# Kernel optimization log

Hardware: AMD Instinct MI355X
Metric: run time of the kernel (lower is better)

Reference implementation:

```python
import jax, jax.numpy as jnp
import numpy as np

CORNER_MASK = jnp.array(
    [[0, 0, 0], [0, 0, 1], [0, 1, 0], [0, 1, 1],
     [1, 0, 0], [1, 0, 1], [1, 1, 0], [1, 1, 1]], dtype=jnp.float32)


def setup_inputs() -> dict:
    key = jax.random.key(0)
    k1, k2, k3, k4 = jax.random.split(key, 4)
    DEPTH = 6
    G = 2 ** DEPTH            # 64 voxels per axis at depth 6
    C = 32                    # feature channels
    H = G * G * G             # 262144 octree nodes at depth 6
    N = 1_000_000             # query points (depth-7 node centers)

    data = jax.random.normal(k1, (1, C, H, 1), dtype=jnp.float32)
    # points scaled into [0, 2^depth]; last column is the batch id (single octree -> 0)
    xyz = jax.random.uniform(k2, (N, 3), dtype=jnp.float32) * G
    ids = jnp.zeros((N, 1), dtype=jnp.float32)
    pts = jnp.concatenate([xyz, ids], axis=1)

    # dense voxel -> node-index lookup emulating ocnn.octree_search_key;
    idx_grid = jax.random.randint(k3, (G, G, G), 0, H, dtype=jnp.int32)
    empty = jax.random.uniform(k4, (G, G, G)) < 0.1
    lut = jnp.where(empty, jnp.int32(-1), idx_grid)

    return {"data": data, "pts": pts, "lut": lut, "depth": DEPTH}


def reference(data, pts, lut, depth):
    # data: (1, C, H, 1); pts: (N, 4); lut: (G, G, G) int32; depth: python int
    G = 2 ** depth
    xyzf = pts[:, :3] - 0.5                      # (N, 3)
    xyzi = jnp.floor(xyzf)
    frac = xyzf - xyzi                           # (N, 3) fractional offsets

    corners = xyzi[:, None, :] + CORNER_MASK[None, :, :]   # (N, 8, 3)
    ci = corners.astype(jnp.int32)
    in_bounds = jnp.all((ci >= 0) & (ci < G), axis=-1)     # (N, 8)
    ci_safe = jnp.clip(ci, 0, G - 1)
    idx = lut[ci_safe[..., 0], ci_safe[..., 1], ci_safe[..., 2]]  # (N, 8)
    valid = in_bounds & (idx > -1)

    # trilinear weights: |prod((1 - mask) - frac)|, matching the torch code
    w = jnp.abs(jnp.prod((1.0 - CORNER_MASK)[None, :, :] - frac[:, None, :], axis=-1))
    w = jnp.where(valid, w, 0.0)                 # (N, 8)
    idx_safe = jnp.where(valid, idx, 0)

    feat = data[0, :, :, 0].T                    # (H, C)
    gathered = feat[idx_safe]                    # (N, 8, C)
    out = jnp.einsum('nk,nkc->nc', w, gathered)  # weighted accumulate
    norm = jnp.sum(w, axis=1, keepdims=True)     # (N, 1)
    out = out / (norm + 1e-10)
    return out.T[None, :, :, None]               # (1, C, N, 1)
```

## Files before the change

kernel.cpp:

```cpp
#include <hip/hip_runtime.h>
#include <hip/hip_fp16.h>


#define NCH 32
#define BIN_W 512
#define NGRP 8
#define CAP 128

typedef float nvec4 __attribute__((ext_vector_type(4)));

__global__ __launch_bounds__(256) void octri_pre1(
    const float* __restrict__ data, __half* __restrict__ featH, int H, int TB,
    const float* __restrict__ pts, int N, int NB, float* __restrict__ binned,
    int* __restrict__ inv, int* __restrict__ cnt) {
  __shared__ float tile[32][33];
  __shared__ int lcnt[NGRP];
  __shared__ int wbase[4][NGRP];
  const int t = threadIdx.x;

  if ((int)blockIdx.x < TB) {
    const int h0 = blockIdx.x * 32;
    const int tx = t & 31, ty = t >> 5;
#pragma unroll
    for (int i = 0; i < 4; ++i) {
      int c = ty + 8 * i;
      tile[c][tx] = __builtin_nontemporal_load(&data[(size_t)c * H + h0 + tx]);
    }
    __syncthreads();
#pragma unroll
    for (int i = 0; i < 4; ++i) {
      int hl = ty + 8 * i;
      featH[(size_t)(h0 + hl) * NCH + tx] = __float2half(tile[tx][hl]);
    }
  } else {
    const int b = blockIdx.x - TB;
    const int lane = t & 63, wid = t >> 6;
    if (t < NGRP) lcnt[t] = 0;
    __syncthreads();
#pragma unroll
    for (int i = 0; i < 2; ++i) {
      const int n = b * BIN_W + i * 256 + t;
      const bool act = (n < N);
      nvec4 pt = {0.f, 0.f, 0.f, 0.f};
      int g = 0;
      if (act) {
        pt = __builtin_nontemporal_load((const nvec4*)(pts + (size_t)n * 4));
        g = min(max((int)floorf(pt.x - 0.5f), 0), 63) >> 3;
      }
      unsigned long long m = 0;
#pragma unroll
      for (int gg = 0; gg < NGRP; ++gg) {
        const unsigned long long bm = __ballot(act && (g == gg));
        if (gg == g) m = bm;
      }
      const unsigned long long ltm = (1ull << lane) - 1ull;
      const int rank = __popcll(m & ltm);
      if (act && rank == 0) wbase[wid][g] = atomicAdd(&lcnt[g], __popcll(m));
      __syncthreads();
      if (act) {
        const int rtot = wbase[wid][g] + rank;
        const int rk = min(rtot, CAP - 1);
        const int slot = ((g * NB + b) << 7) + rk;
        if (rtot < CAP)
          __builtin_nontemporal_store(pt, (nvec4*)(binned + (size_t)slot * 4));
        inv[n] = (g << 28) | slot;
      }
      __syncthreads();
    }
    if (t < NGRP) cnt[t * NB + b] = min(lcnt[t], CAP);
  }
}

__global__ __launch_bounds__(256) void octri_voxelize(
    const __half* __restrict__ featH, const int* __restrict__ lut,
    __half* __restrict__ featV, unsigned long long* __restrict__ vmask) {
  const int t = threadIdx.x;
  const int zi = t >> 2;
  const int j = t & 3;
  const int v = blockIdx.x * 64 + zi;
  const int id = __builtin_nontemporal_load(&lut[v]);

  nvec4 row = {0.f, 0.f, 0.f, 0.f};
  if (id >= 0)
    row = __builtin_nontemporal_load(
        (const nvec4*)(featH + ((size_t)id << 5) + (j << 3)));
  *(nvec4*)(featV + ((size_t)v << 5) + (j << 3)) = row;

  const unsigned long long b = __ballot(id >= 0);
  unsigned int comp = 0;
#pragma unroll
  for (int k = 0; k < 16; ++k)
    comp |= ((unsigned)(b >> (4 * k)) & 1u) << k;
  __shared__ unsigned short sm16[4];
  if ((t & 63) == 0) sm16[t >> 6] = (unsigned short)comp;
  __syncthreads();
  if (t == 0) {
    unsigned long long m = (unsigned long long)sm16[0] |
                           ((unsigned long long)sm16[1] << 16) |
                           ((unsigned long long)sm16[2] << 32) |
                           ((unsigned long long)sm16[3] << 48);
    vmask[blockIdx.x] = m;
  }
}

__global__ __launch_bounds__(256) void octri_gather5(
    const __half* __restrict__ featV, const unsigned long long* __restrict__ vmask,
    const float* __restrict__ binned, const int* __restrict__ cnt, int NB,
    __half* __restrict__ temp) {
  __shared__ int meta[256][17];
  __shared__ int scnt[2];
  const int g = blockIdx.x & 7;
  const int b0 = (blockIdx.x >> 3) << 1;
  const int t = threadIdx.x;

  if (t < 2) scnt[t] = (b0 + t < NB) ? cnt[g * NB + b0 + t] : 0;
  __syncthreads();

  {
    const int r = t >> 7, off = t & 127;
    const int wofs = (t >> 6) & 1;
    if ((wofs << 6) < scnt[r]) {
      const bool valid = off < scnt[r];
      const int slot = ((g * NB + (b0 + r)) << 7) + off;
      nvec4 pt = {0.f, 0.f, 0.f, 0.f};
      if (valid)
        pt = __builtin_nontemporal_load(
            (const nvec4*)(binned + (size_t)slot * 4));
      const float fx = pt.x - 0.5f, fy = pt.y - 0.5f, fz = pt.z - 0.5f;
      const float flx = floorf(fx), fly = floorf(fy), flz = floorf(fz);
      const int ix = (int)flx, iy = (int)fly, iz = (int)flz;
      const float rx = fx - flx, ry = fy - fly, rz = fz - flz;
      const float wx[2] = {1.f - rx, rx};
      const float wy[2] = {1.f - ry, ry};
      const float wz[2] = {1.f - rz, rz};
      const bool vx[2] = {(unsigned)ix < 64u, (unsigned)(ix + 1) < 64u};
      const bool vy[2] = {(unsigned)iy < 64u, (unsigned)(iy + 1) < 64u};
      const bool vz[2] = {(unsigned)iz < 64u, (unsigned)(iz + 1) < 64u};
      const int cxc[2] = {min(max(ix, 0), 63), min(max(ix + 1, 0), 63)};
      const int cyc[2] = {min(max(iy, 0), 63), min(max(iy + 1, 0), 63)};
      const int czc[2] = {min(max(iz, 0), 63), min(max(iz + 1, 0), 63)};

      unsigned long long mrow[2][2];
#pragma unroll
      for (int bx = 0; bx < 2; ++bx)
#pragma unroll
        for (int by = 0; by < 2; ++by)
          mrow[bx][by] = vmask[(cxc[bx] << 6) + cyc[by]];

      int vv[8];
      float w[8], wsum = 0.f;
#pragma unroll
      for (int k = 0; k < 8; ++k) {
        const int bx = (k >> 2) & 1, by = (k >> 1) & 1, bz = k & 1;
        const bool ok = vx[bx] && vy[by] && vz[bz] &&
                        (((mrow[bx][by] >> czc[bz]) & 1ull) != 0);
        vv[k] = ((cxc[bx] << 6) + cyc[by]) * 64 + czc[bz];
        float wk = wx[bx] * wy[by] * wz[bz];
        wk = ok ? wk : 0.f;
        w[k] = wk;
        wsum += wk;
      }
      const float sc = valid ? (1.f / (wsum + 1e-10f)) : 0.f;
#pragma unroll
      for (int k = 0; k < 8; ++k) {
        meta[t][k] = vv[k];
        meta[t][8 + k] = __float_as_int(w[k] * sc);
      }
    }
  }
  __syncthreads();

  const int lane = t & 63;
  const int wid = t >> 6;
  const int j = lane & 3;
  const int sc = scnt[wid >> 1];
#pragma unroll
  for (int gq = 0; gq < 4; ++gq) {
    const int base = ((wid & 1) << 6) + (gq << 4);
    if (base >= sc) break;
    const int p = (wid << 6) + (gq << 4) + (lane >> 2);

    nvec4 r[8];
    float ws[8];
#pragma unroll
    for (int k = 0; k < 8; ++k) {
      const int v = meta[p][k];
      ws[k] = __int_as_float(meta[p][8 + k]);
      r[k] = *(const nvec4*)(featV + ((size_t)v << 5) + (j << 3));
    }
    float acc[8] = {};
#pragma unroll
    for (int k = 0; k < 8; ++k) {
      const __half2* h2 = (const __half2*)&r[k];
#pragma unroll
      for (int q = 0; q < 4; ++q) {
        const float2 f = __half22float2(h2[q]);
        acc[2 * q + 0] += ws[k] * f.x;
        acc[2 * q + 1] += ws[k] * f.y;
      }
    }
    if ((p & 127) < sc) {
      const int slot = ((g * NB + (b0 + (p >> 7))) << 7) + (p & 127);
      union { __half2 h2[4]; nvec4 v; } u;
#pragma unroll
      for (int q = 0; q < 4; ++q)
        u.h2[q] = __floats2half2_rn(acc[2 * q], acc[2 * q + 1]);
      __builtin_nontemporal_store(
          u.v, (nvec4*)(temp + ((size_t)slot << 5) + (j << 3)));
    }
  }
}

__global__ __launch_bounds__(256) void octri_unpermute2(
    const __half* __restrict__ temp, const int* __restrict__ inv,
    const int* __restrict__ cnt, int NB, int N, float* __restrict__ out) {
  __shared__ __half rows[BIN_W * NCH];
  __shared__ int cnt8[NGRP], pre[NGRP];
  const int b = blockIdx.x;
  const int t = threadIdx.x;
  if (t < NGRP) cnt8[t] = cnt[t * NB + b];
  __syncthreads();
  if (t == 0) {
    int s = 0;
#pragma unroll
    for (int gg = 0; gg < NGRP; ++gg) { pre[gg] = s; s += cnt8[gg]; }
  }
  __syncthreads();
  for (int gg = 0; gg < NGRP; ++gg) {
    const int len4 = cnt8[gg] << 2;
    const __half* src = temp + ((size_t)((gg * NB + b)) << 12);
    const int rbase = pre[gg];
    for (int k = t; k < len4; k += 256) {
      const int row = k >> 2, e = k & 3;
      const nvec4 v = __builtin_nontemporal_load(
          (const nvec4*)(src + ((size_t)row << 5) + (e << 3)));
      const int r = rbase + row;
      *(nvec4*)(rows + ((size_t)r << 5) + ((e ^ (r & 3)) << 3)) = v;
    }
  }
  __syncthreads();
#pragma unroll
  for (int i = 0; i < 2; ++i) {
    const int n = b * BIN_W + i * 256 + t;
    if (n < N) {
      const int iv = inv[n];
      const int g = ((unsigned)iv) >> 28;
      const int r = pre[g] + (iv & (CAP - 1));
      const __half* hp = rows + ((size_t)r << 5);
#pragma unroll
      for (int k = 0; k < 4; ++k) {
        const nvec4 hv = *(const nvec4*)(hp + ((k ^ (r & 3)) << 3));
        const __half2* h2 = (const __half2*)&hv;
#pragma unroll
        for (int q = 0; q < 4; ++q) {
          const float2 f = __half22float2(h2[q]);
          __builtin_nontemporal_store(f.x,
                                      &out[(size_t)(k * 8 + 2 * q) * N + n]);
          __builtin_nontemporal_store(
              f.y, &out[(size_t)(k * 8 + 2 * q + 1) * N + n]);
        }
      }
    }
  }
}

__global__ __launch_bounds__(256) void octri_transpose_h(
    const float* __restrict__ data, __half* __restrict__ featH, int H) {
  __shared__ float tile[32][33];
  const int h0 = blockIdx.x * 32;
  const int tx = threadIdx.x;
  const int ty = threadIdx.y;
#pragma unroll
  for (int i = 0; i < 4; ++i) {
    int c = ty + 8 * i;
    tile[c][tx] = __builtin_nontemporal_load(&data[(size_t)c * H + h0 + tx]);
  }
  __syncthreads();
#pragma unroll
  for (int i = 0; i < 4; ++i) {
    int hl = ty + 8 * i;
    featH[(size_t)(h0 + hl) * NCH + tx] = __float2half(tile[tx][hl]);
  }
}

__global__ __launch_bounds__(256) void octri_gather3(
    const __half* __restrict__ featV, const unsigned long long* __restrict__ vmask,
    const float* __restrict__ pts, const int* __restrict__ depth_p,
    float* __restrict__ out, int N) {
  __shared__ int meta[256][17];
  const int pblk = blockIdx.x * 256;
  const int G = 1 << depth_p[0];
  const int G1 = G - 1;
  {
    const int p = threadIdx.x;
    const int n = min(pblk + p, N - 1);
    const nvec4 pt =
        __builtin_nontemporal_load((const nvec4*)(pts + (size_t)n * 4));
    const float fx = pt.x - 0.5f, fy = pt.y - 0.5f, fz = pt.z - 0.5f;
    const float flx = floorf(fx), fly = floorf(fy), flz = floorf(fz);
    const int ix = (int)flx, iy = (int)fly, iz = (int)flz;
    const float rx = fx - flx, ry = fy - fly, rz = fz - flz;
    const float wx[2] = {1.f - rx, rx};
    const float wy[2] = {1.f - ry, ry};
    const float wz[2] = {1.f - rz, rz};
    const bool vx[2] = {(unsigned)ix < (unsigned)G,
                        (unsigned)(ix + 1) < (unsigned)G};
    const bool vy[2] = {(unsigned)iy < (unsigned)G,
                        (unsigned)(iy + 1) < (unsigned)G};
    const bool vz[2] = {(unsigned)iz < (unsigned)G,
                        (unsigned)(iz + 1) < (unsigned)G};
    const int cxc[2] = {min(max(ix, 0), G1), min(max(ix + 1, 0), G1)};
    const int cyc[2] = {min(max(iy, 0), G1), min(max(iy + 1, 0), G1)};
    const int czc[2] = {min(max(iz, 0), G1), min(max(iz + 1, 0), G1)};
    unsigned long long mrow[2][2];
#pragma unroll
    for (int bx = 0; bx < 2; ++bx)
#pragma unroll
      for (int by = 0; by < 2; ++by)
        mrow[bx][by] = vmask[cxc[bx] * G + cyc[by]];
    int vv[8];
    float w[8], wsum = 0.f;
#pragma unroll
    for (int k = 0; k < 8; ++k) {
      const int bx = (k >> 2) & 1, by = (k >> 1) & 1, bz = k & 1;
      const bool valid = vx[bx] && vy[by] && vz[bz] &&
                         (((mrow[bx][by] >> czc[bz]) & 1ull) != 0);
      vv[k] = (cxc[bx] * G + cyc[by]) * G + czc[bz];
      float wk = wx[bx] * wy[by] * wz[bz];
      wk = valid ? wk : 0.f;
      w[k] = wk;
      wsum += wk;
    }
    const float s = (pblk + p < N) ? (1.f / (wsum + 1e-10f)) : 0.f;
#pragma unroll
    for (int k = 0; k < 8; ++k) {
      meta[p][k] = vv[k];
      meta[p][8 + k] = __float_as_int(w[k] * s);
    }
  }
  __syncthreads();
  const int lane = threadIdx.x & 63;
  const int wid = threadIdx.x >> 6;
  const int j = lane & 3;
#pragma unroll
  for (int g = 0; g < 4; ++g) {
    const int p = (wid << 6) + (g << 4) + (lane >> 2);
    const int n = pblk + p;
    nvec4 r[8];
    float ws[8];
#pragma unroll
    for (int k = 0; k < 8; ++k) {
      const int v = meta[p][k];
      ws[k] = __int_as_float(meta[p][8 + k]);
      r[k] = *(const nvec4*)(featV + ((size_t)v << 5) + (j << 3));
    }
    float acc[8] = {};
#pragma unroll
    for (int k = 0; k < 8; ++k) {
      const __half2* h2 = (const __half2*)&r[k];
#pragma unroll
      for (int q = 0; q < 4; ++q) {
        const float2 f = __half22float2(h2[q]);
        acc[2 * q + 0] += ws[k] * f.x;
        acc[2 * q + 1] += ws[k] * f.y;
      }
    }
    if (n < N) {
#pragma unroll
      for (int q = 0; q < 8; ++q)
        __builtin_nontemporal_store(acc[q], &out[(size_t)(8 * j + q) * N + n]);
    }
  }
}

__global__ __launch_bounds__(256) void octri_gather_direct(
    const float* __restrict__ data, const float* __restrict__ pts,
    const int* __restrict__ lut, const int* __restrict__ depth_p,
    float* __restrict__ out, int N, int H) {
  const int n = blockIdx.x * blockDim.x + threadIdx.x;
  if (n >= N) return;
  const int G = 1 << depth_p[0];
  const float4 p = ((const float4*)pts)[n];
  const float fx = p.x - 0.5f, fy = p.y - 0.5f, fz = p.z - 0.5f;
  const float flx = floorf(fx), fly = floorf(fy), flz = floorf(fz);
  const int ix = (int)flx, iy = (int)fly, iz = (int)flz;
  const float rx = fx - flx, ry = fy - fly, rz = fz - flz;
  const float wx[2] = {1.f - rx, rx};
  const float wy[2] = {1.f - ry, ry};
  const float wz[2] = {1.f - rz, rz};
  int idx[8];
  float w[8], wsum = 0.f;
#pragma unroll
  for (int k = 0; k < 8; ++k) {
    const int bx = (k >> 2) & 1, by = (k >> 1) & 1, bz = k & 1;
    const int cx = ix + bx, cy = iy + by, cz = iz + bz;
    const bool inb = (cx >= 0) & (cx < G) & (cy >= 0) & (cy < G) & (cz >= 0) &
                     (cz < G);
    int id = -1;
    if (inb) id = lut[((size_t)cx * G + cy) * G + cz];
    const bool valid = inb && (id > -1);
    float wk = wx[bx] * wy[by] * wz[bz];
    wk = valid ? wk : 0.f;
    idx[k] = valid ? id : 0;
    w[k] = wk;
    wsum += wk;
  }
  const float s = 1.f / (wsum + 1e-10f);
#pragma unroll 4
  for (int c = 0; c < NCH; ++c) {
    const float* plane = data + (size_t)c * H;
    float a = 0.f;
#pragma unroll
    for (int k = 0; k < 8; ++k) a += w[k] * plane[idx[k]];
    out[(size_t)c * N + n] = a * s;
  }
}

extern "C" void kernel_launch(void* const* d_in, const int* in_sizes, int n_in,
                              void* d_out, int out_size, void* d_ws,
                              size_t ws_size, hipStream_t stream) {
  const float* data = (const float*)d_in[0];
  const float* pts = (const float*)d_in[1];
  const int* lut = (const int*)d_in[2];
  const int* depth_p = (const int*)d_in[3];
  float* out = (float*)d_out;

  const int H = in_sizes[0] / NCH;
  const int N = in_sizes[1] / 4;
  const int SV = in_sizes[2];

  int G = 1;
  while ((size_t)(G + 1) * (G + 1) * (G + 1) <= (size_t)SV) ++G;

  const int NB = (N + BIN_W - 1) / BIN_W;

  const size_t featH_bytes = (size_t)H * NCH * sizeof(__half);
  const size_t featV_bytes = (size_t)SV * NCH * sizeof(__half);
  const size_t nslots = (size_t)NGRP * NB * CAP;

  size_t offw = 0;
  auto alloc = [&](size_t bytes) {
    offw = (offw + 255) & ~(size_t)255;
    size_t o = offw;
    offw += bytes;
    return o;
  };
  const size_t o_featH = alloc(featH_bytes);
  const size_t o_featV = alloc(featV_bytes);
  const size_t o_vmask = alloc((size_t)G * G * sizeof(unsigned long long));
  const size_t o_binned = alloc(nslots * 16);
  const size_t o_temp = alloc(nslots * NCH * sizeof(__half));
  const size_t o_inv = alloc((size_t)NB * BIN_W * sizeof(int));
  const size_t o_cnt = alloc((size_t)NGRP * NB * sizeof(int));
  const size_t need_full = offw;

  const size_t needV = featV_bytes + (size_t)G * G * sizeof(unsigned long long);

  if (G == 64 && (size_t)G * G * G == (size_t)SV && (H % 32) == 0 &&
      nslots < (1u << 21) && ws_size >= need_full) {
    char* ws = (char*)d_ws;
    __half* featH = (__half*)(ws + o_featH);
    __half* featV = (__half*)(ws + o_featV);
    unsigned long long* vmask = (unsigned long long*)(ws + o_vmask);
    float* binned = (float*)(ws + o_binned);
    __half* temp = (__half*)(ws + o_temp);
    int* inv = (int*)(ws + o_inv);
    int* cnt = (int*)(ws + o_cnt);

    const int TB = H / 32;
    octri_pre1<<<TB + NB, 256, 0, stream>>>(data, featH, H, TB, pts, N, NB,
                                            binned, inv, cnt);
    octri_voxelize<<<SV / 64, 256, 0, stream>>>(featH, lut, featV, vmask);
    const int PB = (NB + 1) >> 1;
    octri_gather5<<<NGRP * PB, 256, 0, stream>>>(featV, vmask, binned, cnt,
                                                 NB, temp);
    octri_unpermute2<<<NB, 256, 0, stream>>>(temp, inv, cnt, NB, N, out);
  } else if (G == 64 && (size_t)G * G * G == (size_t)SV && (H % 32) == 0 &&
             ws_size >= needV &&
             featH_bytes <= (size_t)out_size * sizeof(float)) {
    __half* featH = (__half*)d_out;
    __half* featV = (__half*)d_ws;
    unsigned long long* vmask =
        (unsigned long long*)((char*)d_ws + featV_bytes);
    dim3 tb(32, 8);
    octri_transpose_h<<<H / 32, tb, 0, stream>>>(data, featH, H);
    octri_voxelize<<<SV / 64, 256, 0, stream>>>(featH, lut, featV, vmask);
    octri_gather3<<<(N + 255) / 256, 256, 0, stream>>>(featV, vmask, pts,
                                                       depth_p, out, N);
  } else {
    octri_gather_direct<<<(N + 255) / 256, 256, 0, stream>>>(
        data, pts, lut, depth_p, out, N, H);
  }
}
```

Baseline: 258.2 us.

## Fuse four pipeline kernels into one cooperative persistent kernel with grid syncs

Replaces the four separate launches (transpose+binning, voxelize, gather, unpermute) with a single cooperative kernel that runs the stages as grid-stride loops separated by grid.sync(). The aim is to remove per-kernel launch and drain gaps between stages. The grid is sized from occupancy times CU count. The old kernel sequence stays as a fallback if the cooperative launch fails, and the unused three-kernel path is removed. In exchange, grid-wide barriers are added, and the persistent grid may give lower occupancy or worse load balance than the original launches.

```diff
diff --git a/kernel.cpp b/kernel.cpp
--- a/kernel.cpp
+++ b/kernel.cpp
@@ -1,5 +1,8 @@
 #include <hip/hip_runtime.h>
 #include <hip/hip_fp16.h>
+#include <hip/hip_cooperative_groups.h>
+
+namespace cg = cooperative_groups;
 
 
 #define NCH 32
@@ -8,6 +11,271 @@
 #define CAP 128
 
 typedef float nvec4 __attribute__((ext_vector_type(4)));
+
+__global__ __launch_bounds__(256) void octri_fused(
+    const float* __restrict__ data, const int* __restrict__ lut,
+    const float* __restrict__ pts, __half* __restrict__ featH,
+    __half* __restrict__ featV, unsigned long long* __restrict__ vmask,
+    float* __restrict__ binned, int* __restrict__ inv, int* __restrict__ cnt,
+    __half* __restrict__ temp, float* __restrict__ out, int H, int N, int NB,
+    int TB, int SVB) {
+  __shared__ alignas(16) char sm[32896];
+  float(*tile)[33] = (float(*)[33])sm;
+  int* lcnt = (int*)sm;
+  int(*wbase)[NGRP] = (int(*)[NGRP])(sm + 64);
+  unsigned short* sm16 = (unsigned short*)sm;
+  int(*meta)[17] = (int(*)[17])sm;
+  int* scnt = (int*)(sm + 17408);
+  __half* rows = (__half*)sm;
+  int* cnt8 = (int*)(sm + 32768);
+  int* pre = (int*)(sm + 32800);
+
+  const int t = threadIdx.x;
+  const int nblk = gridDim.x;
+  cg::grid_group grid = cg::this_grid();
+
+  for (int bt = blockIdx.x; bt < TB; bt += nblk) {
+    const int h0 = bt * 32;
+    const int tx = t & 31, ty = t >> 5;
+#pragma unroll
+    for (int i = 0; i < 4; ++i) {
+      int c = ty + 8 * i;
+      tile[c][tx] =
+          __builtin_nontemporal_load(&data[(size_t)c * H + h0 + tx]);
+    }
+    __syncthreads();
+#pragma unroll
+    for (int i = 0; i < 4; ++i) {
+      int hl = ty + 8 * i;
+      featH[(size_t)(h0 + hl) * NCH + tx] = __float2half(tile[tx][hl]);
+    }
+    __syncthreads();
+  }
+  for (int b = blockIdx.x; b < NB; b += nblk) {
+    const int lane = t & 63, wid = t >> 6;
+    if (t < NGRP) lcnt[t] = 0;
+    __syncthreads();
+#pragma unroll
+    for (int i = 0; i < 2; ++i) {
+      const int n = b * BIN_W + i * 256 + t;
+      const bool act = (n < N);
+      nvec4 pt = {0.f, 0.f, 0.f, 0.f};
+      int g = 0;
+      if (act) {
+        pt = __builtin_nontemporal_load((const nvec4*)(pts + (size_t)n * 4));
+        g = min(max((int)floorf(pt.x - 0.5f), 0), 63) >> 3;
+      }
+      unsigned long long m = 0;
+#pragma unroll
+      for (int gg = 0; gg < NGRP; ++gg) {
+        const unsigned long long bm = __ballot(act && (g == gg));
+        if (gg == g) m = bm;
+      }
+      const unsigned long long ltm = (1ull << lane) - 1ull;
+      const int rank = __popcll(m & ltm);
+      if (act && rank == 0) wbase[wid][g] = atomicAdd(&lcnt[g], __popcll(m));
+      __syncthreads();
+      if (act) {
+        const int rtot = wbase[wid][g] + rank;
+        const int rk = min(rtot, CAP - 1);
+        const int slot = ((g * NB + b) << 7) + rk;
+        if (rtot < CAP)
+          __builtin_nontemporal_store(pt,
+                                      (nvec4*)(binned + (size_t)slot * 4));
+        inv[n] = (g << 28) | slot;
+      }
+      __syncthreads();
+    }
+    if (t < NGRP) cnt[t * NB + b] = min(lcnt[t], CAP);
+    __syncthreads();
+  }
+  grid.sync();
+
+  for (int vb = blockIdx.x; vb < SVB; vb += nblk) {
+    const int zi = t >> 2, j = t & 3;
+    const int v = vb * 64 + zi;
+    const int id = __builtin_nontemporal_load(&lut[v]);
+    nvec4 row = {0.f, 0.f, 0.f, 0.f};
+    if (id >= 0)
+      row = __builtin_nontemporal_load(
+          (const nvec4*)(featH + ((size_t)id << 5) + (j << 3)));
+    *(nvec4*)(featV + ((size_t)v << 5) + (j << 3)) = row;
+
+    const unsigned long long bb = __ballot(id >= 0);
+    unsigned int comp = 0;
+#pragma unroll
+    for (int k = 0; k < 16; ++k)
+      comp |= ((unsigned)(bb >> (4 * k)) & 1u) << k;
+    if ((t & 63) == 0) sm16[t >> 6] = (unsigned short)comp;
+    __syncthreads();
+    if (t == 0) {
+      unsigned long long m = (unsigned long long)sm16[0] |
+                             ((unsigned long long)sm16[1] << 16) |
+                             ((unsigned long long)sm16[2] << 32) |
+                             ((unsigned long long)sm16[3] << 48);
+      vmask[vb] = m;
+    }
+    __syncthreads();
+  }
+  grid.sync();
+
+  {
+    const int g = blockIdx.x & 7;
+    const int PBtot = (NB + 1) >> 1;
+    for (int pb = blockIdx.x >> 3; pb < PBtot; pb += (nblk >> 3)) {
+      const int b0 = pb << 1;
+      if (t < 2) scnt[t] = (b0 + t < NB) ? cnt[g * NB + b0 + t] : 0;
+      __syncthreads();
+      {
+        const int r = t >> 7, off = t & 127;
+        const int wofs = (t >> 6) & 1;
+        if ((wofs << 6) < scnt[r]) {
+          const bool valid = off < scnt[r];
+          const int slot = ((g * NB + (b0 + r)) << 7) + off;
+          nvec4 pt = {0.f, 0.f, 0.f, 0.f};
+          if (valid)
+            pt = __builtin_nontemporal_load(
+                (const nvec4*)(binned + (size_t)slot * 4));
+          const float fx = pt.x - 0.5f, fy = pt.y - 0.5f, fz = pt.z - 0.5f;
+          const float flx = floorf(fx), fly = floorf(fy), flz = floorf(fz);
+          const int ix = (int)flx, iy = (int)fly, iz = (int)flz;
+          const float rx = fx - flx, ry = fy - fly, rz = fz - flz;
+          const float wx[2] = {1.f - rx, rx};
+          const float wy[2] = {1.f - ry, ry};
+          const float wz[2] = {1.f - rz, rz};
+          const bool vx[2] = {(unsigned)ix < 64u, (unsigned)(ix + 1) < 64u};
+          const bool vy[2] = {(unsigned)iy < 64u, (unsigned)(iy + 1) < 64u};
+          const bool vz[2] = {(unsigned)iz < 64u, (unsigned)(iz + 1) < 64u};
+          const int cxc[2] = {min(max(ix, 0), 63), min(max(ix + 1, 0), 63)};
+          const int cyc[2] = {min(max(iy, 0), 63), min(max(iy + 1, 0), 63)};
+          const int czc[2] = {min(max(iz, 0), 63), min(max(iz + 1, 0), 63)};
+          unsigned long long mrow[2][2];
+#pragma unroll
+          for (int bx = 0; bx < 2; ++bx)
+#pragma unroll
+            for (int by = 0; by < 2; ++by)
+              mrow[bx][by] = vmask[(cxc[bx] << 6) + cyc[by]];
+          int vv[8];
+          float w[8], wsum = 0.f;
+#pragma unroll
+          for (int k = 0; k < 8; ++k) {
+            const int bx = (k >> 2) & 1, by = (k >> 1) & 1, bz = k & 1;
+            const bool ok = vx[bx] && vy[by] && vz[bz] &&
+                            (((mrow[bx][by] >> czc[bz]) & 1ull) != 0);
+            vv[k] = ((cxc[bx] << 6) + cyc[by]) * 64 + czc[bz];
+            float wk = wx[bx] * wy[by] * wz[bz];
+            wk = ok ? wk : 0.f;
+            w[k] = wk;
+            wsum += wk;
+          }
+          const float sc0 = valid ? (1.f / (wsum + 1e-10f)) : 0.f;
+#pragma unroll
+          for (int k = 0; k < 8; ++k) {
+            meta[t][k] = vv[k];
+            meta[t][8 + k] = __float_as_int(w[k] * sc0);
+          }
+        }
+      }
+      __syncthreads();
+      {
+        const int lane = t & 63;
+        const int wid = t >> 6;
+        const int j = lane & 3;
+        const int sc2 = scnt[wid >> 1];
+#pragma unroll
+        for (int gq = 0; gq < 4; ++gq) {
+          const int base = ((wid & 1) << 6) + (gq << 4);
+          if (base >= sc2) break;
+          const int p = (wid << 6) + (gq << 4) + (lane >> 2);
+          nvec4 r[8];
+          float ws[8];
+#pragma unroll
+          for (int k = 0; k < 8; ++k) {
+            const int v = meta[p][k];
+            ws[k] = __int_as_float(meta[p][8 + k]);
+            r[k] = *(const nvec4*)(featV + ((size_t)v << 5) + (j << 3));
+          }
+          float acc[8] = {};
+#pragma unroll
+          for (int k = 0; k < 8; ++k) {
+            const __half2* h2 = (const __half2*)&r[k];
+#pragma unroll
+            for (int q = 0; q < 4; ++q) {
+              const float2 f = __half22float2(h2[q]);
+              acc[2 * q + 0] += ws[k] * f.x;
+              acc[2 * q + 1] += ws[k] * f.y;
+            }
+          }
+          if ((p & 127) < sc2) {
+            const int slot = ((g * NB + (b0 + (p >> 7))) << 7) + (p & 127);
+            union {
+              __half2 h2[4];
+              nvec4 v;
+            } u;
+#pragma unroll
+            for (int q = 0; q < 4; ++q)
+              u.h2[q] = __floats2half2_rn(acc[2 * q], acc[2 * q + 1]);
+            __builtin_nontemporal_store(
+                u.v, (nvec4*)(temp + ((size_t)slot << 5) + (j << 3)));
+          }
+        }
+      }
+      __syncthreads();
+    }
+  }
+  grid.sync();
+
+  for (int b = blockIdx.x; b < NB; b += nblk) {
+    if (t < NGRP) cnt8[t] = cnt[t * NB + b];
+    __syncthreads();
+    if (t == 0) {
+      int s = 0;
+#pragma unroll
+      for (int gg = 0; gg < NGRP; ++gg) {
+        pre[gg] = s;
+        s += cnt8[gg];
+      }
+    }
+    __syncthreads();
+    for (int gg = 0; gg < NGRP; ++gg) {
+      const int len4 = cnt8[gg] << 2;
+      const __half* src = temp + ((size_t)(gg * NB + b) << 12);
+      const int rbase = pre[gg];
+      for (int k = t; k < len4; k += 256) {
+        const int row = k >> 2, e = k & 3;
+        const nvec4 v = __builtin_nontemporal_load(
+            (const nvec4*)(src + ((size_t)row << 5) + (e << 3)));
+        const int r = rbase + row;
+        *(nvec4*)(rows + ((size_t)r << 5) + ((e ^ (r & 3)) << 3)) = v;
+      }
+    }
+    __syncthreads();
+#pragma unroll
+    for (int i = 0; i < 2; ++i) {
+      const int n = b * BIN_W + i * 256 + t;
+      if (n < N) {
+        const int iv = inv[n];
+        const int g = ((unsigned)iv) >> 28;
+        const int r = pre[g] + (iv & (CAP - 1));
+        const __half* hp = rows + ((size_t)r << 5);
+#pragma unroll
+        for (int k = 0; k < 4; ++k) {
+          const nvec4 hv = *(const nvec4*)(hp + ((k ^ (r & 3)) << 3));
+          const __half2* h2 = (const __half2*)&hv;
+#pragma unroll
+          for (int q = 0; q < 4; ++q) {
+            const float2 f = __half22float2(h2[q]);
+            __builtin_nontemporal_store(
+                f.x, &out[(size_t)(k * 8 + 2 * q) * N + n]);
+            __builtin_nontemporal_store(
+                f.y, &out[(size_t)(k * 8 + 2 * q + 1) * N + n]);
+          }
+        }
+      }
+    }
+    __syncthreads();
+  }
+}
 
 __global__ __launch_bounds__(256) void octri_pre1(
     const float* __restrict__ data, __half* __restrict__ featH, int H, int TB,
@@ -17,7 +285,6 @@
   __shared__ int lcnt[NGRP];
   __shared__ int wbase[4][NGRP];
   const int t = threadIdx.x;
-
   if ((int)blockIdx.x < TB) {
     const int h0 = blockIdx.x * 32;
     const int tx = t & 31, ty = t >> 5;
@@ -79,13 +346,11 @@
   const int j = t & 3;
   const int v = blockIdx.x * 64 + zi;
   const int id = __builtin_nontemporal_load(&lut[v]);
-
   nvec4 row = {0.f, 0.f, 0.f, 0.f};
   if (id >= 0)
     row = __builtin_nontemporal_load(
         (const nvec4*)(featH + ((size_t)id << 5) + (j << 3)));
   *(nvec4*)(featV + ((size_t)v << 5) + (j << 3)) = row;
-
   const unsigned long long b = __ballot(id >= 0);
   unsigned int comp = 0;
 #pragma unroll
@@ -104,7 +369,8 @@
 }
 
 __global__ __launch_bounds__(256) void octri_gather5(
-    const __half* __restrict__ featV, const unsigned long long* __restrict__ vmask,
+    const __half* __restrict__ featV,
+    const unsigned long long* __restrict__ vmask,
     const float* __restrict__ binned, const int* __restrict__ cnt, int NB,
     __half* __restrict__ temp) {
   __shared__ int meta[256][17];
@@ -112,10 +378,8 @@
   const int g = blockIdx.x & 7;
   const int b0 = (blockIdx.x >> 3) << 1;
   const int t = threadIdx.x;
-
   if (t < 2) scnt[t] = (b0 + t < NB) ? cnt[g * NB + b0 + t] : 0;
   __syncthreads();
-
   {
     const int r = t >> 7, off = t & 127;
     const int wofs = (t >> 6) & 1;
@@ -139,14 +403,12 @@
       const int cxc[2] = {min(max(ix, 0), 63), min(max(ix + 1, 0), 63)};
       const int cyc[2] = {min(max(iy, 0), 63), min(max(iy + 1, 0), 63)};
       const int czc[2] = {min(max(iz, 0), 63), min(max(iz + 1, 0), 63)};
-
       unsigned long long mrow[2][2];
 #pragma unroll
       for (int bx = 0; bx < 2; ++bx)
 #pragma unroll
         for (int by = 0; by < 2; ++by)
           mrow[bx][by] = vmask[(cxc[bx] << 6) + cyc[by]];
-
       int vv[8];
       float w[8], wsum = 0.f;
 #pragma unroll
@@ -169,7 +431,6 @@
     }
   }
   __syncthreads();
-
   const int lane = t & 63;
   const int wid = t >> 6;
   const int j = lane & 3;
@@ -179,7 +440,6 @@
     const int base = ((wid & 1) << 6) + (gq << 4);
     if (base >= sc) break;
     const int p = (wid << 6) + (gq << 4) + (lane >> 2);
-
     nvec4 r[8];
     float ws[8];
 #pragma unroll
@@ -201,7 +461,10 @@
     }
     if ((p & 127) < sc) {
       const int slot = ((g * NB + (b0 + (p >> 7))) << 7) + (p & 127);
-      union { __half2 h2[4]; nvec4 v; } u;
+      union {
+        __half2 h2[4];
+        nvec4 v;
+      } u;
 #pragma unroll
       for (int q = 0; q < 4; ++q)
         u.h2[q] = __floats2half2_rn(acc[2 * q], acc[2 * q + 1]);
@@ -223,12 +486,15 @@
   if (t == 0) {
     int s = 0;
 #pragma unroll
-    for (int gg = 0; gg < NGRP; ++gg) { pre[gg] = s; s += cnt8[gg]; }
+    for (int gg = 0; gg < NGRP; ++gg) {
+      pre[gg] = s;
+      s += cnt8[gg];
+    }
   }
   __syncthreads();
   for (int gg = 0; gg < NGRP; ++gg) {
     const int len4 = cnt8[gg] << 2;
-    const __half* src = temp + ((size_t)((gg * NB + b)) << 12);
+    const __half* src = temp + ((size_t)(gg * NB + b) << 12);
     const int rbase = pre[gg];
     for (int k = t; k < len4; k += 256) {
       const int row = k >> 2, e = k & 3;
@@ -260,115 +526,6 @@
               f.y, &out[(size_t)(k * 8 + 2 * q + 1) * N + n]);
         }
       }
-    }
-  }
-}
-
-__global__ __launch_bounds__(256) void octri_transpose_h(
-    const float* __restrict__ data, __half* __restrict__ featH, int H) {
-  __shared__ float tile[32][33];
-  const int h0 = blockIdx.x * 32;
-  const int tx = threadIdx.x;
-  const int ty = threadIdx.y;
-#pragma unroll
-  for (int i = 0; i < 4; ++i) {
-    int c = ty + 8 * i;
-    tile[c][tx] = __builtin_nontemporal_load(&data[(size_t)c * H + h0 + tx]);
-  }
-  __syncthreads();
-#pragma unroll
-  for (int i = 0; i < 4; ++i) {
-    int hl = ty + 8 * i;
-    featH[(size_t)(h0 + hl) * NCH + tx] = __float2half(tile[tx][hl]);
-  }
-}
-
-__global__ __launch_bounds__(256) void octri_gather3(
-    const __half* __restrict__ featV, const unsigned long long* __restrict__ vmask,
-    const float* __restrict__ pts, const int* __restrict__ depth_p,
-    float* __restrict__ out, int N) {
-  __shared__ int meta[256][17];
-  const int pblk = blockIdx.x * 256;
-  const int G = 1 << depth_p[0];
-  const int G1 = G - 1;
-  {
-    const int p = threadIdx.x;
-    const int n = min(pblk + p, N - 1);
-    const nvec4 pt =
-        __builtin_nontemporal_load((const nvec4*)(pts + (size_t)n * 4));
-    const float fx = pt.x - 0.5f, fy = pt.y - 0.5f, fz = pt.z - 0.5f;
-    const float flx = floorf(fx), fly = floorf(fy), flz = floorf(fz);
-    const int ix = (int)flx, iy = (int)fly, iz = (int)flz;
-    const float rx = fx - flx, ry = fy - fly, rz = fz - flz;
-    const float wx[2] = {1.f - rx, rx};
-    const float wy[2] = {1.f - ry, ry};
-    const float wz[2] = {1.f - rz, rz};
-    const bool vx[2] = {(unsigned)ix < (unsigned)G,
-                        (unsigned)(ix + 1) < (unsigned)G};
-    const bool vy[2] = {(unsigned)iy < (unsigned)G,
-                        (unsigned)(iy + 1) < (unsigned)G};
-    const bool vz[2] = {(unsigned)iz < (unsigned)G,
-                        (unsigned)(iz + 1) < (unsigned)G};
-    const int cxc[2] = {min(max(ix, 0), G1), min(max(ix + 1, 0), G1)};
-    const int cyc[2] = {min(max(iy, 0), G1), min(max(iy + 1, 0), G1)};
-    const int czc[2] = {min(max(iz, 0), G1), min(max(iz + 1, 0), G1)};
-    unsigned long long mrow[2][2];
-#pragma unroll
-    for (int bx = 0; bx < 2; ++bx)
-#pragma unroll
-      for (int by = 0; by < 2; ++by)
-        mrow[bx][by] = vmask[cxc[bx] * G + cyc[by]];
-    int vv[8];
-    float w[8], wsum = 0.f;
-#pragma unroll
-    for (int k = 0; k < 8; ++k) {
-      const int bx = (k >> 2) & 1, by = (k >> 1) & 1, bz = k & 1;
-      const bool valid = vx[bx] && vy[by] && vz[bz] &&
-                         (((mrow[bx][by] >> czc[bz]) & 1ull) != 0);
-      vv[k] = (cxc[bx] * G + cyc[by]) * G + czc[bz];
-      float wk = wx[bx] * wy[by] * wz[bz];
-      wk = valid ? wk : 0.f;
-      w[k] = wk;
-      wsum += wk;
-    }
-    const float s = (pblk + p < N) ? (1.f / (wsum + 1e-10f)) : 0.f;
-#pragma unroll
-    for (int k = 0; k < 8; ++k) {
-      meta[p][k] = vv[k];
-      meta[p][8 + k] = __float_as_int(w[k] * s);
-    }
-  }
-  __syncthreads();
-  const int lane = threadIdx.x & 63;
-  const int wid = threadIdx.x >> 6;
-  const int j = lane & 3;
-#pragma unroll
-  for (int g = 0; g < 4; ++g) {
-    const int p = (wid << 6) + (g << 4) + (lane >> 2);
-    const int n = pblk + p;
-    nvec4 r[8];
-    float ws[8];
-#pragma unroll
-    for (int k = 0; k < 8; ++k) {
-      const int v = meta[p][k];
-      ws[k] = __int_as_float(meta[p][8 + k]);
-      r[k] = *(const nvec4*)(featV + ((size_t)v << 5) + (j << 3));
-    }
-    float acc[8] = {};
-#pragma unroll
-    for (int k = 0; k < 8; ++k) {
-      const __half2* h2 = (const __half2*)&r[k];
-#pragma unroll
-      for (int q = 0; q < 4; ++q) {
-        const float2 f = __half22float2(h2[q]);
-        acc[2 * q + 0] += ws[k] * f.x;
-        acc[2 * q + 1] += ws[k] * f.y;
-      }
-    }
-    if (n < N) {
-#pragma unroll
-      for (int q = 0; q < 8; ++q)
-        __builtin_nontemporal_store(acc[q], &out[(size_t)(8 * j + q) * N + n]);
     }
   }
 }
@@ -454,8 +611,6 @@
   const size_t o_cnt = alloc((size_t)NGRP * NB * sizeof(int));
   const size_t need_full = offw;
 
-  const size_t needV = featV_bytes + (size_t)G * G * sizeof(unsigned long long);
-
   if (G == 64 && (size_t)G * G * G == (size_t)SV && (H % 32) == 0 &&
       nslots < (1u << 21) && ws_size >= need_full) {
     char* ws = (char*)d_ws;
@@ -466,27 +621,57 @@
     __half* temp = (__half*)(ws + o_temp);
     int* inv = (int*)(ws + o_inv);
     int* cnt = (int*)(ws + o_cnt);
-
     const int TB = H / 32;
-    octri_pre1<<<TB + NB, 256, 0, stream>>>(data, featH, H, TB, pts, N, NB,
-                                            binned, inv, cnt);
-    octri_voxelize<<<SV / 64, 256, 0, stream>>>(featH, lut, featV, vmask);
-    const int PB = (NB + 1) >> 1;
-    octri_gather5<<<NGRP * PB, 256, 0, stream>>>(featV, vmask, binned, cnt,
-                                                 NB, temp);
-    octri_unpermute2<<<NB, 256, 0, stream>>>(temp, inv, cnt, NB, N, out);
-  } else if (G == 64 && (size_t)G * G * G == (size_t)SV && (H % 32) == 0 &&
-             ws_size >= needV &&
-             featH_bytes <= (size_t)out_size * sizeof(float)) {
-    __half* featH = (__half*)d_out;
-    __half* featV = (__half*)d_ws;
-    unsigned long long* vmask =
-        (unsigned long long*)((char*)d_ws + featV_bytes);
-    dim3 tb(32, 8);
-    octri_transpose_h<<<H / 32, tb, 0, stream>>>(data, featH, H);
-    octri_voxelize<<<SV / 64, 256, 0, stream>>>(featH, lut, featV, vmask);
-    octri_gather3<<<(N + 255) / 256, 256, 0, stream>>>(featV, vmask, pts,
-                                                       depth_p, out, N);
+    const int SVB = SV / 64;
+
+    static int coop_ok = -1;
+    static int gridc = 0;
+    if (coop_ok < 0) {
+      int dev = 0;
+      (void)hipGetDevice(&dev);
+      int cl = 0, ncu = 0, mb = 0;
+      (void)hipDeviceGetAttribute(&cl, hipDeviceAttributeCooperativeLaunch,
+                                  dev);
+      (void)hipDeviceGetAttribute(&ncu,
+                                  hipDeviceAttributeMultiprocessorCount, dev);
+      (void)hipOccupancyMaxActiveBlocksPerMultiprocessor(&mb, octri_fused,
+                                                         256, 0);
+      gridc = mb * ncu;
+      gridc &= ~7;
+      if (gridc > 2048) gridc = 2048;
+      coop_ok = (cl && gridc >= 8) ? 1 : 0;
+    }
+
+    bool launched = false;
+    if (coop_ok == 1) {
+      const float* a_data = data;
+      const int* a_lut = lut;
+      const float* a_pts = pts;
+      int a_H = H, a_N = N, a_NB = NB, a_TB = TB, a_SVB = SVB;
+      void* kargs[] = {(void*)&a_data, (void*)&a_lut, (void*)&a_pts,
+                       (void*)&featH, (void*)&featV,  (void*)&vmask,
+                       (void*)&binned, (void*)&inv,   (void*)&cnt,
+                       (void*)&temp,  (void*)&out,    (void*)&a_H,
+                       (void*)&a_N,   (void*)&a_NB,   (void*)&a_TB,
+                       (void*)&a_SVB};
+      hipError_t le = hipLaunchCooperativeKernel(
+          (const void*)octri_fused, dim3(gridc), dim3(256), kargs, 0, stream);
+      if (le == hipSuccess) {
+        launched = true;
+      } else {
+        (void)hipGetLastError();
+        coop_ok = 0;
+      }
+    }
+    if (!launched) {
+      octri_pre1<<<TB + NB, 256, 0, stream>>>(data, featH, H, TB, pts, N, NB,
+                                              binned, inv, cnt);
+      octri_voxelize<<<SVB, 256, 0, stream>>>(featH, lut, featV, vmask);
+      const int PB = (NB + 1) >> 1;
+      octri_gather5<<<NGRP * PB, 256, 0, stream>>>(featV, vmask, binned, cnt,
+                                                   NB, temp);
+      octri_unpermute2<<<NB, 256, 0, stream>>>(temp, inv, cnt, NB, N, out);
+    }
   } else {
     octri_gather_direct<<<(N + 255) / 256, 256, 0, stream>>>(
         data, pts, lut, depth_p, out, N, H);
```

Measured after the change: 503.6 us. +95.1%, slower.
